# Optimization experiments

Hardware: AMD Instinct MI355X
Metric: run time of the kernel (lower is better)

Reference implementation:

```python
import jax, jax.numpy as jnp
import numpy as np

# SCOFFCell config (version=1, share_inp=True, step_att=True, LSTM, no rel-memory)
NUM_HIDDEN = 8      # number of object files (blocks)
SINGLE = 128        # single_hidden_size = hidden // num_hidden
N_TEMPLATES = 4     # schemata
COMM_HEADS = 4
D_KC = 32           # comm attn d_k = d_v
D_KI = 64           # input attn d_k
TOPK = 5            # topkval: active blocks
TAU = 0.5           # gumbel-softmax temperature for template selection
BS, NUM_INPUTS, INPUT_SIZE = 2048, 8, 128
HIDDEN = NUM_HIDDEN * SINGLE


def setup_inputs() -> dict:
    key = jax.random.key(0)
    ks = jax.random.split(key, 20)
    s = 0.05
    n = lambda k, shape, sc=s: jax.random.normal(k, shape, jnp.float32) * sc
    return {
        'inp': jax.random.normal(ks[0], (BS, NUM_INPUTS, INPUT_SIZE), jnp.float32),
        'hx': jax.random.normal(ks[1], (BS, HIDDEN), jnp.float32),
        'cx': jax.random.normal(ks[2], (BS, HIDDEN), jnp.float32),
        # input attention (shared across blocks, skip_write -> no output proj)
        'Wq_i': n(ks[3], (SINGLE, D_KI)),
        'Wk_i': n(ks[4], (INPUT_SIZE, D_KI)),
        'Wv_i': n(ks[5], (INPUT_SIZE, SINGLE)),
        # communication attention
        'Wq_c': n(ks[6], (SINGLE, COMM_HEADS * D_KC)),
        'Wk_c': n(ks[7], (SINGLE, COMM_HEADS * D_KC)),
        'Wv_c': n(ks[8], (SINGLE, COMM_HEADS * D_KC)),
        'Wf_c': n(ks[9], (COMM_HEADS * D_KC, SINGLE)),
        'bf_c': jnp.zeros((SINGLE,), jnp.float32),
        'Wg_c': n(ks[10], (COMM_HEADS * D_KC, SINGLE)),
        'bg_c': jnp.zeros((SINGLE,), jnp.float32),
        # SharedBlockLSTM: n_templates LSTMCells (torch gate order i,f,g,o)
        'W_ih': n(ks[11], (N_TEMPLATES, 4 * SINGLE, SINGLE)),
        'W_hh': n(ks[12], (N_TEMPLATES, 4 * SINGLE, SINGLE)),
        'b_ih': jnp.zeros((N_TEMPLATES, 4 * SINGLE), jnp.float32),
        'b_hh': jnp.zeros((N_TEMPLATES, 4 * SINGLE), jnp.float32),
        # template read/write keys
        'W_read': n(ks[13], (SINGLE, 16)),
        'W_write': n(ks[14], (N_TEMPLATES, SINGLE, 16)),
    }


def _scoff_forward(inp, hx, cx, Wq_i, Wk_i, Wv_i, Wq_c, Wk_c, Wv_c, Wf_c, bf_c,
                   Wg_c, bg_c, W_ih, W_hh, b_ih, b_hh, W_read, W_write):
    bs = inp.shape[0]
    k, sh = NUM_HIDDEN, SINGLE
    # ---- input attention: each block's hx chunk queries [slots ++ null-slot] ----
    kv = jnp.concatenate([inp, jnp.zeros_like(inp[:, :1])], axis=1)  # [bs, n_in+1, d_in]
    q = hx.reshape(bs, k, sh)
    qs = q @ Wq_i                                     # [bs, k, d_ki]
    ksl = kv @ Wk_i                                   # [bs, n_in+1, d_ki]
    vs = kv @ Wv_i                                    # [bs, n_in+1, sh]
    iatt = jax.nn.softmax(jnp.einsum('bkd,bnd->bkn', qs, ksl) / jnp.sqrt(jnp.float32(D_KI)), axis=-1)
    inp_use = jnp.einsum('bkn,bnd->bkd', iatt, vs).reshape(bs, k * sh)
    # ---- top-k block mask: zero the (k - topkval) blocks with largest iatt[:,:,0] ----
    n_drop = k - TOPK
    _, drop_idx = jax.lax.top_k(iatt[:, :, 0], n_drop)
    new_mask = jnp.ones((bs, k), inp.dtype).at[jnp.arange(bs)[:, None], drop_idx].set(0.0)
    mask_b = jax.lax.stop_gradient(new_mask)          # mask.detach()
    block_mask = mask_b[:, :, None]                   # [bs, k, 1]
    mask = jnp.repeat(block_mask, sh, axis=2).reshape(bs, k * sh)
    # ---- SharedBlockLSTM: run all templates, gumbel-ST select per block ----
    x = inp_use.reshape(bs * k, sh)
    h = hx.reshape(bs * k, sh)
    c = cx.reshape(bs * k, sh)
    gates = (jnp.einsum('ni,mgi->nmg', x, W_ih) + jnp.einsum('ni,mgi->nmg', h, W_hh)
             + b_ih + b_hh)                           # [N, m, 4*sh]
    i_g, f_g, g_g, o_g = jnp.split(gates, 4, axis=-1)
    c_t = jax.nn.sigmoid(f_g) * c[:, None, :] + jax.nn.sigmoid(i_g) * jnp.tanh(g_g)  # [N, m, sh]
    h_t = jax.nn.sigmoid(o_g) * jnp.tanh(c_t)
    h_read = h @ W_read                               # [N, 16]
    write_key = jnp.einsum('nms,msd->nmd', h_t, W_write)  # [N, m, 16]
    logits = jnp.einsum('nd,nmd->nm', h_read, write_key)
    gkey = jax.random.fold_in(jax.random.key(0), 12345)
    gumb = jax.random.gumbel(gkey, logits.shape, logits.dtype)
    y_soft = jax.nn.softmax((logits + gumb) / TAU, axis=-1)
    y_hard = jax.nn.one_hot(jnp.argmax(y_soft, axis=-1), N_TEMPLATES, dtype=y_soft.dtype)
    att = y_soft + jax.lax.stop_gradient(y_hard - y_soft)  # straight-through gumbel
    hx_new = jnp.einsum('nm,nms->ns', att, h_t).reshape(bs, k * sh)
    cx_new = jnp.einsum('nm,nms->ns', att, c_t).reshape(bs, k * sh)
    temp_att = att.reshape(bs, k, N_TEMPLATES)
    # ---- communication attention over blocks (blocked_grad masking) ----
    hb = hx_new.reshape(bs, k, sh)
    m3 = mask.reshape(bs, k, sh)
    hbg = m3 * hb + jax.lax.stop_gradient((1.0 - m3) * hb)  # fwd identity, bwd grad*mask
    heads = lambda t, W: (t @ W).reshape(bs, k, COMM_HEADS, D_KC).transpose(0, 2, 1, 3)
    qc, kc, vc = heads(hbg, Wq_c), heads(hbg, Wk_c), heads(hbg, Wv_c)
    catt = jax.nn.softmax(jnp.einsum('bhqd,bhkd->bhqk', qc, kc) / jnp.sqrt(jnp.float32(D_KC)), axis=-1)
    o = jnp.einsum('bhqk,bhkd->bhqd', catt, vc).transpose(0, 2, 1, 3).reshape(bs, k, COMM_HEADS * D_KC)
    comm = jax.nn.sigmoid(o @ Wg_c + bg_c) * jnp.tanh(o @ Wf_c + bf_c)  # gated residual update
    hx_new = (hb + comm).reshape(bs, k * sh)
    # ---- write back only active blocks ----
    hx_out = mask * hx_new + (1.0 - mask) * hx
    cx_out = mask * cx_new + (1.0 - mask) * cx
    return hx_out, cx_out, mask, block_mask, temp_att


def reference(inp, hx, cx, Wq_i, Wk_i, Wv_i, Wq_c, Wk_c, Wv_c, Wf_c, bf_c,
              Wg_c, bg_c, W_ih, W_hh, b_ih, b_hh, W_read, W_write):
    return _scoff_forward(inp, hx, cx, Wq_i, Wk_i, Wv_i, Wq_c, Wk_c, Wv_c, Wf_c,
                          bf_c, Wg_c, bg_c, W_ih, W_hh, b_ih, b_hh, W_read, W_write)
```

## Files before the change

### kernel.cpp

```cpp
#include <hip/hip_runtime.h>
#include <hip/hip_bf16.h>
#include <stdint.h>

typedef __hip_bfloat16 bf16;
typedef _Float16 half_t;
typedef __attribute__((ext_vector_type(8))) _Float16 half8;
typedef __attribute__((ext_vector_type(4))) float float4v;

struct TF2 { unsigned a, b; };
__host__ __device__ constexpr unsigned rotl32(unsigned v, int r) {
  return (v << r) | (v >> (32 - r));
}
__host__ __device__ constexpr TF2 tf2x32(unsigned k0, unsigned k1, unsigned x0, unsigned x1) {
  unsigned ks2 = k0 ^ k1 ^ 0x1BD11BDAu;
  x0 += k0; x1 += k1;
  const int ra[4] = {13, 15, 26, 6};
  const int rb[4] = {17, 29, 16, 24};
  for (int i = 0; i < 4; i++) { x0 += x1; x1 = rotl32(x1, ra[i]); x1 ^= x0; }
  x0 += k1; x1 += ks2 + 1u;
  for (int i = 0; i < 4; i++) { x0 += x1; x1 = rotl32(x1, rb[i]); x1 ^= x0; }
  x0 += ks2; x1 += k0 + 2u;
  for (int i = 0; i < 4; i++) { x0 += x1; x1 = rotl32(x1, ra[i]); x1 ^= x0; }
  x0 += k0; x1 += k1 + 3u;
  for (int i = 0; i < 4; i++) { x0 += x1; x1 = rotl32(x1, rb[i]); x1 ^= x0; }
  x0 += k1; x1 += ks2 + 4u;
  for (int i = 0; i < 4; i++) { x0 += x1; x1 = rotl32(x1, ra[i]); x1 ^= x0; }
  x0 += ks2; x1 += k0 + 5u;
  return TF2{x0, x1};
}
constexpr unsigned GK0 = tf2x32(0u, 0u, 0u, 12345u).a;
constexpr unsigned GK1 = tf2x32(0u, 0u, 0u, 12345u).b;

__device__ __forceinline__ float gumbel_at(unsigned j) {
  TF2 r = tf2x32(GK0, GK1, 0u, j);
  unsigned bits = r.a ^ r.b;
  float u = __uint_as_float((bits >> 9) | 0x3f800000u) - 1.0f;
  u = fmaxf(1.17549435e-38f, u + 1.17549435e-38f);
  return -logf(-logf(u));
}

__device__ __forceinline__ float sigm(float x) { return 1.0f / (1.0f + expf(-x)); }

#define MFMA16(a, b, c) __builtin_amdgcn_mfma_f32_16x16x32_f16((a), (b), (c), 0, 0, 0)

constexpr int GH  = 0;
constexpr int GL  = 524288;
constexpr int WWH = 1048576;
constexpr int WWL = 1056768;
constexpr int CQ  = 1064960;
constexpr int CF  = 1114112;
constexpr int CG  = 1130496;
constexpr int WS_HALF_TOTAL = 1146880;
constexpr size_t WS_FLAG_OFF = (size_t)WS_HALF_TOTAL * 2;
constexpr size_t WS_NEED     = WS_FLAG_OFF + 64;

constexpr size_t F_GH  = 0;
constexpr size_t F_GL  = 524288;
constexpr size_t F_WWH = 1048576;
constexpr size_t F_WWL = 1056768;
constexpr size_t F_CQ  = 1064960;
constexpr size_t F_XH  = 1146880;
constexpr size_t F_XL  = 5341184;
constexpr size_t F_HB  = 9535488;
constexpr size_t F_END = 11632640;
constexpr size_t G_HREAD = 0;
constexpr size_t G_MASK8 = 262144;
constexpr size_t G_FLAG  = 278528;
constexpr size_t WS2_NEED = F_END * 2 + (G_FLAG + 16) * 4;

__global__ void k_detect(const void* inp, int* flag) {
  __shared__ int bad;
  if (threadIdx.x == 0) bad = 0;
  __syncthreads();
  const unsigned short* u = (const unsigned short*)inp;
  for (int i = threadIdx.x; i < 1024; i += 256) {
    float v = __uint_as_float(((unsigned)u[i]) << 16);
    if (!(fabsf(v) < 64.f)) atomicOr(&bad, 1);
  }
  __syncthreads();
  if (threadIdx.x == 0) *flag = bad ? 0 : 1;
}

__global__ __launch_bounds__(256)
void k_wsplit2(const int* __restrict__ flag,
               const float* __restrict__ W_ih, const float* __restrict__ W_hh,
               const float* __restrict__ W_write,
               const float* __restrict__ Wq_c, const float* __restrict__ Wk_c,
               const float* __restrict__ Wv_c, const float* __restrict__ Wf_c,
               const float* __restrict__ Wg_c, half_t* __restrict__ ws) {
  if (*flag != 0) return;
  int tid = blockIdx.x * 256 + threadIdx.x;
  if (tid < 65536) {
    int m = tid >> 14, nt = (tid >> 9) & 31, ks = (tid >> 6) & 7, lane = tid & 63;
    int n = m * 512 + nt * 16 + (lane & 15);
    int kb = ks * 32 + (lane >> 4) * 8;
    half8 hi, lo;
#pragma unroll
    for (int j = 0; j < 8; j++) {
      int k = kb + j;
      float w = (k < 128) ? W_ih[n * 128 + k] : W_hh[n * 128 + (k - 128)];
      half_t h = (half_t)w;
      hi[j] = h; lo[j] = (half_t)(w - (float)h);
    }
    *reinterpret_cast<half8*>(ws + F_GH + (size_t)tid * 8) = hi;
    *reinterpret_cast<half8*>(ws + F_GL + (size_t)tid * 8) = lo;
  } else if (tid < 73728) {
    int j = tid - 65536; int md = j >> 7, s = j & 127; int m = md >> 4, d = md & 15;
    float w = W_write[(m * 128 + s) * 16 + d];
    half_t h = (half_t)w;
    ws[F_WWH + j] = h;
    ws[F_WWL + j] = (half_t)(w - (float)h);
  } else if (tid < 83968) {
    int u = tid - 73728;
    int which = u >> 11, r8 = u & 2047;
    int col = r8 >> 4, k8 = r8 & 15;
    const float* Wsel = which == 0 ? Wq_c : which == 1 ? Wk_c :
                        which == 2 ? Wv_c : which == 3 ? Wf_c : Wg_c;
    half8 v;
#pragma unroll
    for (int j = 0; j < 8; j++) v[j] = (half_t)Wsel[(k8 * 8 + j) * 128 + col];
    *reinterpret_cast<half8*>(ws + F_CQ + (size_t)which * 16384 + col * 128 + k8 * 8) = v;
  }
}

__global__ __launch_bounds__(256)
void kA(const int* __restrict__ flag,
        const float* __restrict__ inp, const float* __restrict__ hx,
        const float* __restrict__ Wq_i, const float* __restrict__ Wk_i,
        const float* __restrict__ Wv_i, const float* __restrict__ W_read,
        half_t* __restrict__ xh, half_t* __restrict__ xl,
        float* __restrict__ hread, float* __restrict__ mask8,
        float* __restrict__ out_mask, float* __restrict__ out_bm)
{
  if (*flag != 0) return;
  const int t = threadIdx.x;
  const int n0 = blockIdx.x * 16, gbase = n0 * 128;
  __shared__ __align__(16) float inps[2048], hxs[2048], vsb[2048];
  __shared__ float qsb[1088], kslb[1088];
  __shared__ float Xf[2112];
  __shared__ float attb[160];
  __shared__ float m8_[16];

  for (int idx = t; idx < 512; idx += 256) {
    *reinterpret_cast<float4*>(&hxs[idx * 4]) =
        *reinterpret_cast<const float4*>(hx + gbase + idx * 4);
    *reinterpret_cast<float4*>(&inps[idx * 4]) =
        *reinterpret_cast<const float4*>(inp + gbase + idx * 4);
  }
  __syncthreads();
  for (int idx = t; idx < 1024; idx += 256) {
    int k16 = idx >> 6, d = idx & 63;
    float aq = 0.f, ak = 0.f;
#pragma unroll 8
    for (int i = 0; i < 128; i++) {
      aq += hxs[k16 * 128 + i]  * Wq_i[i * 64 + d];
      ak += inps[k16 * 128 + i] * Wk_i[i * 64 + d];
    }
    qsb[k16 * 68 + d] = aq; kslb[k16 * 68 + d] = ak;
  }
  for (int idx = t; idx < 2048; idx += 256) {
    int n16 = idx >> 7, j = idx & 127;
    float a = 0.f;
#pragma unroll 8
    for (int i = 0; i < 128; i++) a += inps[n16 * 128 + i] * Wv_i[i * 128 + j];
    vsb[idx] = a;
  }
  {
    int n16 = t >> 4, d = t & 15;
    float a = 0.f;
#pragma unroll 8
    for (int i = 0; i < 128; i++) a += hxs[n16 * 128 + i] * W_read[i * 16 + d];
    hread[(size_t)(n0 + n16) * 16 + d] = a;
  }
  __syncthreads();
  if (t < 128) {
    int b2 = t >> 6, k = (t >> 3) & 7, n = t & 7;
    float sc = 0.f;
#pragma unroll
    for (int d = 0; d < 64; d++)
      sc += qsb[(b2 * 8 + k) * 68 + d] * kslb[(b2 * 8 + n) * 68 + d];
    attb[b2 * 72 + k * 9 + n] = sc * 0.125f;
  } else if (t < 144) {
    int u = t - 128, b2 = u >> 3, k = u & 7;
    attb[b2 * 72 + k * 9 + 8] = 0.f;
  }
  __syncthreads();
  if (t < 16) {
    int b2 = t >> 3, k = t & 7;
    float* row = &attb[b2 * 72 + k * 9];
    float mx = row[0];
    for (int n = 1; n < 9; n++) mx = fmaxf(mx, row[n]);
    float e[9], ssum = 0.f;
    for (int n = 0; n < 9; n++) { e[n] = expf(row[n] - mx); ssum += e[n]; }
    for (int n = 0; n < 9; n++) row[n] = e[n] / ssum;
  }
  __syncthreads();
  if (t < 2) {
    bool taken[8] = {};
    for (int dd = 0; dd < 3; dd++) {
      int bi = 0; float bv = -1e30f;
      for (int k = 0; k < 8; k++) {
        float v = attb[t * 72 + k * 9 + 0];
        if (!taken[k] && v > bv) { bv = v; bi = k; }
      }
      taken[bi] = true;
    }
    for (int k = 0; k < 8; k++) m8_[t * 8 + k] = taken[k] ? 0.f : 1.f;
  }
  __syncthreads();
  for (int idx = t; idx < 2048; idx += 256) {
    int n16 = idx >> 7, j = idx & 127, b2 = n16 >> 3, k = n16 & 7;
    float a = 0.f;
#pragma unroll
    for (int n = 0; n < 8; n++) a += attb[b2 * 72 + k * 9 + n] * vsb[(b2 * 8 + n) * 128 + j];
    Xf[n16 * 132 + j] = a;
    out_mask[gbase + idx] = m8_[n16];
  }
  if (t < 16) { out_bm[n0 + t] = m8_[t]; mask8[n0 + t] = m8_[t]; }
  __syncthreads();
  for (int u = t; u < 512; u += 256) {
    int ks = u >> 6, lane = u & 63, c15 = lane & 15, qd = lane >> 4;
    int kb = ks * 32 + qd * 8;
    half8 hi, lo;
#pragma unroll
    for (int j = 0; j < 8; j++) {
      int k = kb + j;
      float v = (k < 128) ? Xf[c15 * 132 + k] : hxs[c15 * 128 + (k - 128)];
      half_t h = (half_t)v;
      hi[j] = h; lo[j] = (half_t)(v - (float)h);
    }
    size_t off = ((size_t)(blockIdx.x * 8 + ks) * 64 + lane) * 8;
    *reinterpret_cast<half8*>(xh + off) = hi;
    *reinterpret_cast<half8*>(xl + off) = lo;
  }
}

__global__ __launch_bounds__(512, 2)
void kB(const int* __restrict__ flag, const half_t* __restrict__ wsp,
        const float* __restrict__ cx,
        const float* __restrict__ b_ih, const float* __restrict__ b_hh,
        const float* __restrict__ hread, const float* __restrict__ mask8,
        half_t* __restrict__ hbout, float* __restrict__ out_cx,
        float* __restrict__ out_ta)
{
  if (*flag != 0) return;
  const int t = threadIdx.x, lane = t & 63, w = t >> 6;
  const int m = w >> 1, sh = w & 1;
  const int c15 = lane & 15, qd = lane >> 4;
  const int n0 = blockIdx.x * 32;

  __shared__ __align__(16) half_t hth[32 * 520];
  __shared__ __align__(16) half_t htl[32 * 520];
  __shared__ float wks[2048];
  __shared__ float zb[128];
  __shared__ float m8s[32];
  __shared__ int msh[32];

  if (t < 32) m8s[t] = mask8[n0 + t];

  float4v acc[16][2];
#pragma unroll
  for (int ct = 0; ct < 16; ct++)
#pragma unroll
    for (int mt = 0; mt < 2; mt++) acc[ct][mt] = (float4v){0.f, 0.f, 0.f, 0.f};

  const half_t* xh = wsp + F_XH;
  const half_t* xl = wsp + F_XL;
  for (int ks = 0; ks < 8; ks++) {
    half8 ah[2], al[2];
#pragma unroll
    for (int mt = 0; mt < 2; mt++) {
      size_t aoff = ((size_t)((blockIdx.x * 2 + mt) * 8 + ks) * 64 + lane) * 8;
      ah[mt] = *reinterpret_cast<const half8*>(xh + aoff);
      al[mt] = *reinterpret_cast<const half8*>(xl + aoff);
    }
#pragma unroll
    for (int ct = 0; ct < 16; ct++) {
      int nt = (ct >> 2) * 8 + sh * 4 + (ct & 3);
      size_t boff = ((size_t)((m * 32 + nt) * 8 + ks) * 64 + lane) * 8;
      half8 bh = *reinterpret_cast<const half8*>(wsp + F_GH + boff);
      half8 bl = *reinterpret_cast<const half8*>(wsp + F_GL + boff);
#pragma unroll
      for (int mt = 0; mt < 2; mt++) {
        acc[ct][mt] = MFMA16(ah[mt], bh, acc[ct][mt]);
        acc[ct][mt] = MFMA16(ah[mt], bl, acc[ct][mt]);
        acc[ct][mt] = MFMA16(al[mt], bh, acc[ct][mt]);
      }
    }
  }
  float ccr[4][2][4];
#pragma unroll
  for (int c4 = 0; c4 < 4; c4++) {
    int s = sh * 64 + c4 * 16 + c15;
    float bi = b_ih[m * 512 + s]       + b_hh[m * 512 + s];
    float bf = b_ih[m * 512 + 128 + s] + b_hh[m * 512 + 128 + s];
    float bg = b_ih[m * 512 + 256 + s] + b_hh[m * 512 + 256 + s];
    float bo = b_ih[m * 512 + 384 + s] + b_hh[m * 512 + 384 + s];
#pragma unroll
    for (int mt = 0; mt < 2; mt++) {
#pragma unroll
      for (int rg = 0; rg < 4; rg++) {
        int row = mt * 16 + qd * 4 + rg;
        float iv = acc[c4][mt][rg]      + bi;
        float fv = acc[4 + c4][mt][rg]  + bf;
        float gv = acc[8 + c4][mt][rg]  + bg;
        float ov = acc[12 + c4][mt][rg] + bo;
        float cxv = cx[(size_t)(n0 + row) * 128 + s];
        float cc = sigm(fv) * cxv + sigm(iv) * tanhf(gv);
        float hh = sigm(ov) * tanhf(cc);
        ccr[c4][mt][rg] = cc;
        half_t hhi = (half_t)hh;
        hth[row * 520 + m * 128 + s] = hhi;
        htl[row * 520 + m * 128 + s] = (half_t)(hh - (float)hhi);
      }
    }
  }
  __syncthreads();
  {
    float4v wa = (float4v){0.f, 0.f, 0.f, 0.f};
    const half_t* Wh = wsp + F_WWH + (m * 16 + c15) * 128 + qd * 8;
    const half_t* Wl = wsp + F_WWL + (m * 16 + c15) * 128 + qd * 8;
    const half_t* Hh = &hth[(sh * 16 + c15) * 520 + m * 128 + qd * 8];
    const half_t* Hl = &htl[(sh * 16 + c15) * 520 + m * 128 + qd * 8];
#pragma unroll
    for (int ks = 0; ks < 4; ks++) {
      half8 ahf = *reinterpret_cast<const half8*>(Hh + ks * 32);
      half8 alf = *reinterpret_cast<const half8*>(Hl + ks * 32);
      half8 bhf = *reinterpret_cast<const half8*>(Wh + ks * 32);
      half8 blf = *reinterpret_cast<const half8*>(Wl + ks * 32);
      wa = MFMA16(ahf, bhf, wa);
      wa = MFMA16(ahf, blf, wa);
      wa = MFMA16(alf, bhf, wa);
    }
#pragma unroll
    for (int rg = 0; rg < 4; rg++)
      wks[m * 512 + (sh * 16 + qd * 4 + rg) * 16 + c15] = wa[rg];
  }
  __syncthreads();
  if (t < 128) {
    int row = t >> 2, mm = t & 3;
    float lg = 0.f;
#pragma unroll
    for (int d = 0; d < 16; d++)
      lg += hread[(size_t)(n0 + row) * 16 + d] * wks[mm * 512 + row * 16 + d];
    zb[t] = lg + gumbel_at((unsigned)((n0 + row) * 4 + mm));
  }
  __syncthreads();
  if (t < 32) {
    int ms = 0; float best = zb[t * 4];
#pragma unroll
    for (int mm = 1; mm < 4; mm++)
      if (zb[t * 4 + mm] > best) { best = zb[t * 4 + mm]; ms = mm; }
    msh[t] = ms;
#pragma unroll
    for (int mm = 0; mm < 4; mm++)
      out_ta[(size_t)(n0 + t) * 4 + mm] = (mm == ms) ? 1.0f : 0.0f;
  }
  __syncthreads();
#pragma unroll
  for (int c4 = 0; c4 < 4; c4++) {
    int s = sh * 64 + c4 * 16 + c15;
#pragma unroll
    for (int mt = 0; mt < 2; mt++) {
#pragma unroll
      for (int rg = 0; rg < 4; rg++) {
        int row = mt * 16 + qd * 4 + rg;
        if (msh[row] == m) {
          float co = (m8s[row] != 0.f) ? ccr[c4][mt][rg]
                                       : cx[(size_t)(n0 + row) * 128 + s];
          out_cx[(size_t)(n0 + row) * 128 + s] = co;
        }
      }
    }
  }
  for (int idx = t; idx < 4096; idx += 512) {
    int r = idx >> 7, s = idx & 127;
    hbout[(size_t)(n0 + r) * 128 + s] = hth[r * 520 + msh[r] * 128 + s];
  }
}

__global__ __launch_bounds__(256)
void kC(const int* __restrict__ flag, const half_t* __restrict__ wsp,
        const half_t* __restrict__ hbin, const float* __restrict__ mask8,
        const float* __restrict__ hx,
        const float* __restrict__ bf_c, const float* __restrict__ bg_c,
        float* __restrict__ out_hx)
{
  if (*flag != 0) return;
  const int t = threadIdx.x;
  const int n0 = blockIdx.x * 16;
  const int lane = t & 63, wv = t >> 6;
  const int col15 = lane & 15, quad = lane >> 4;

  __shared__ __align__(16) half_t hbF[2176], qcF[2176], kcF[2176], vcF[2176], oF[2176];
  __shared__ float attb[512];
  __shared__ float m8s[16];

  {
    int r = t >> 4, c8 = t & 15;
    *reinterpret_cast<half8*>(&hbF[r * 136 + c8 * 8]) =
        *reinterpret_cast<const half8*>(hbin + (size_t)(n0 + r) * 128 + c8 * 8);
  }
  if (t < 16) m8s[t] = mask8[n0 + t];
  __syncthreads();

  if (wv < 3) {
    float4v pacc[8];
#pragma unroll
    for (int ct = 0; ct < 8; ct++) pacc[ct] = (float4v){0.f, 0.f, 0.f, 0.f};
    const half_t* Bp = wsp + F_CQ + wv * 16384 + col15 * 128 + quad * 8;
    const half_t* Ap = &hbF[col15 * 136 + quad * 8];
#pragma unroll
    for (int ks = 0; ks < 4; ks++) {
      half8 a = *reinterpret_cast<const half8*>(Ap + ks * 32);
#pragma unroll
      for (int ct = 0; ct < 8; ct++) {
        half8 b = *reinterpret_cast<const half8*>(Bp + ct * 2048 + ks * 32);
        pacc[ct] = MFMA16(a, b, pacc[ct]);
      }
    }
    half_t* dst = (wv == 0) ? qcF : (wv == 1) ? kcF : vcF;
#pragma unroll
    for (int ct = 0; ct < 8; ct++)
#pragma unroll
      for (int rg = 0; rg < 4; rg++)
        dst[(quad * 4 + rg) * 136 + ct * 16 + col15] = (half_t)pacc[ct][rg];
  }
  __syncthreads();

  if (t < 64) {
    int b2 = t >> 5, h = (t >> 3) & 3, q = t & 7;
    float sc[8];
#pragma unroll
    for (int kq = 0; kq < 8; kq++) {
      float a = 0.f;
#pragma unroll
      for (int d = 0; d < 32; d++)
        a += (float)qcF[(b2 * 8 + q) * 136 + h * 32 + d] *
             (float)kcF[(b2 * 8 + kq) * 136 + h * 32 + d];
      sc[kq] = a * 0.17677669529663688110f;
    }
    float mx = sc[0];
#pragma unroll
    for (int kq = 1; kq < 8; kq++) mx = fmaxf(mx, sc[kq]);
    float e[8], ssum = 0.f;
#pragma unroll
    for (int kq = 0; kq < 8; kq++) { e[kq] = expf(sc[kq] - mx); ssum += e[kq]; }
#pragma unroll
    for (int kq = 0; kq < 8; kq++)
      attb[((b2 * 4 + h) * 8 + q) * 8 + kq] = e[kq] / ssum;
  }
  __syncthreads();

  for (int idx = t; idx < 2048; idx += 256) {
    int r = idx >> 7, cn = idx & 127, b2 = r >> 3, q = r & 7, h = cn >> 5;
    float a = 0.f;
#pragma unroll
    for (int kq = 0; kq < 8; kq++)
      a += attb[((b2 * 4 + h) * 8 + q) * 8 + kq] * (float)vcF[(b2 * 8 + kq) * 136 + cn];
    oF[r * 136 + cn] = (half_t)a;
  }
  __syncthreads();

  {
    float4v fa[2], ga[2];
#pragma unroll
    for (int tt = 0; tt < 2; tt++) {
      fa[tt] = (float4v){0.f, 0.f, 0.f, 0.f};
      ga[tt] = (float4v){0.f, 0.f, 0.f, 0.f};
    }
    const half_t* Ao = &oF[col15 * 136 + quad * 8];
    const half_t* Bf = wsp + F_CQ + 3 * 16384 + (wv * 32 + col15) * 128 + quad * 8;
    const half_t* Bg = wsp + F_CQ + 4 * 16384 + (wv * 32 + col15) * 128 + quad * 8;
#pragma unroll
    for (int ks = 0; ks < 4; ks++) {
      half8 a = *reinterpret_cast<const half8*>(Ao + ks * 32);
#pragma unroll
      for (int tt = 0; tt < 2; tt++) {
        half8 bfv = *reinterpret_cast<const half8*>(Bf + tt * 2048 + ks * 32);
        half8 bgv = *reinterpret_cast<const half8*>(Bg + tt * 2048 + ks * 32);
        fa[tt] = MFMA16(a, bfv, fa[tt]);
        ga[tt] = MFMA16(a, bgv, ga[tt]);
      }
    }
#pragma unroll
    for (int tt = 0; tt < 2; tt++) {
      int col = wv * 32 + tt * 16 + col15;
      float bfb = bf_c[col], bgb = bg_c[col];
#pragma unroll
      for (int rg = 0; rg < 4; rg++) {
        int row = quad * 4 + rg;
        float af = fa[tt][rg] + bfb;
        float ag = ga[tt][rg] + bgb;
        float comm = sigm(ag) * tanhf(af);
        float hbv = (float)hbF[row * 136 + col];
        float hv = (m8s[row] != 0.f) ? (hbv + comm)
                                     : hx[(size_t)(n0 + row) * 128 + col];
        out_hx[(size_t)(n0 + row) * 128 + col] = hv;
      }
    }
  }
}

__global__ __launch_bounds__(256)
void k_wsplit(const float* __restrict__ W_ih, const float* __restrict__ W_hh,
              const float* __restrict__ W_write,
              const float* __restrict__ Wq_c, const float* __restrict__ Wk_c,
              const float* __restrict__ Wv_c, const float* __restrict__ Wf_c,
              const float* __restrict__ Wg_c, half_t* __restrict__ ws) {
  int i = blockIdx.x * 256 + threadIdx.x;
  if (i < 524288) {
    int n = i >> 8, k = i & 255;
    int m = n >> 9, g = n & 511;
    float w = (k < 128) ? W_ih[(m * 512 + g) * 128 + k]
                        : W_hh[(m * 512 + g) * 128 + (k - 128)];
    half_t h = (half_t)w;
    ws[GH + i] = h;
    ws[GL + i] = (half_t)(w - (float)h);
  } else if (i < 532480) {
    int j = i - 524288; int md = j >> 7, s = j & 127; int m = md >> 4, d = md & 15;
    float w = W_write[(m * 128 + s) * 16 + d];
    half_t h = (half_t)w;
    ws[WWH + j] = h;
    ws[WWL + j] = (half_t)(w - (float)h);
  } else if (i < 614400) {
    int j = i - 532480; int which = j >> 14, r = j & 16383;
    int col = r >> 7, k = r & 127;
    const float* Wsel = which == 0 ? Wq_c : which == 1 ? Wk_c :
                        which == 2 ? Wv_c : which == 3 ? Wf_c : Wg_c;
    ws[CQ + which * 16384 + r] = (half_t)Wsel[k * 128 + col];
  }
}

__global__ __launch_bounds__(256)
void k_scoff_mfma(const int* __restrict__ flag, const half_t* __restrict__ wsp,
                  const float* __restrict__ inp, const float* __restrict__ hx,
                  const float* __restrict__ cx,
                  const float* __restrict__ Wq_i, const float* __restrict__ Wk_i,
                  const float* __restrict__ Wv_i,
                  const float* __restrict__ bf_c, const float* __restrict__ bg_c,
                  const float* __restrict__ b_ih, const float* __restrict__ b_hh,
                  const float* __restrict__ W_read,
                  float* __restrict__ out_hx, float* __restrict__ out_cx,
                  float* __restrict__ out_mask, float* __restrict__ out_bm,
                  float* __restrict__ out_ta)
{
  if (*flag != 0) return;

  const int t = threadIdx.x;
  const int n0 = blockIdx.x * 16, gbase = n0 * 128;
  const int lane = t & 63, wv = t >> 6;
  const int col15 = lane & 15, quad = lane >> 4;

  __shared__ __align__(16) float hxs[2048];
  __shared__ __align__(16) float cxs[2048];
  __shared__ __align__(16) float vsb[2048];
  __shared__ float qsb[1088], kslb[1088];
  __shared__ __align__(16) half_t sXh[16 * 264];
  __shared__ __align__(16) half_t sXl[16 * 264];
  __shared__ __align__(16) half_t hth[16 * 520];
  __shared__ __align__(16) half_t htl[16 * 520];
  __shared__ __align__(16) half_t cts[16 * 512];
  __shared__ float wks[1024];
  __shared__ __align__(16) half_t hbF[16 * 136];
  __shared__ __align__(16) half_t oF[16 * 136];
  __shared__ __align__(16) half_t qcF[16 * 136];
  __shared__ __align__(16) half_t kcF[16 * 136];
  __shared__ __align__(16) half_t vcF[16 * 136];
  __shared__ float attb[512];
  __shared__ float hrs_[256];
  __shared__ float zbuf[64];
  __shared__ float m8_[16];
  __shared__ int   msh_[16];

  for (int idx = t; idx < 512; idx += 256) {
    *reinterpret_cast<float4*>(&hxs[idx * 4]) =
        *reinterpret_cast<const float4*>(hx + gbase + idx * 4);
    *reinterpret_cast<float4*>(&cxs[idx * 4]) =
        *reinterpret_cast<const float4*>(cx + gbase + idx * 4);
  }
  {
    __shared__ __align__(16) float inps[2048];
    for (int idx = t; idx < 512; idx += 256)
      *reinterpret_cast<float4*>(&inps[idx * 4]) =
          *reinterpret_cast<const float4*>(inp + gbase + idx * 4);
    __syncthreads();
    for (int idx = t; idx < 1024; idx += 256) {
      int k16 = idx >> 6, d = idx & 63;
      float aq = 0.f, ak = 0.f;
#pragma unroll 8
      for (int i = 0; i < 128; i++) {
        aq += hxs[k16 * 128 + i]  * Wq_i[i * 64 + d];
        ak += inps[k16 * 128 + i] * Wk_i[i * 64 + d];
      }
      qsb[k16 * 68 + d] = aq; kslb[k16 * 68 + d] = ak;
    }
    for (int idx = t; idx < 2048; idx += 256) {
      int n16 = idx >> 7, j = idx & 127;
      float a = 0.f;
#pragma unroll 8
      for (int i = 0; i < 128; i++) a += inps[n16 * 128 + i] * Wv_i[i * 128 + j];
      vsb[idx] = a;
    }
  }
  {
    int n16 = t >> 4, d = t & 15;
    float a = 0.f;
#pragma unroll 8
    for (int i = 0; i < 128; i++) a += hxs[n16 * 128 + i] * W_read[i * 16 + d];
    hrs_[t] = a;
  }
  for (int idx = t; idx < 2048; idx += 256) {
    int r = idx >> 7, i = idx & 127;
    float v = hxs[r * 128 + i];
    half_t hh = (half_t)v;
    sXh[r * 264 + 128 + i] = hh;
    sXl[r * 264 + 128 + i] = (half_t)(v - (float)hh);
  }
  __syncthreads();

  if (t < 128) {
    int b2 = t >> 6, k = (t >> 3) & 7, n = t & 7;
    float sc = 0.f;
#pragma unroll
    for (int d = 0; d < 64; d++)
      sc += qsb[(b2 * 8 + k) * 68 + d] * kslb[(b2 * 8 + n) * 68 + d];
    attb[b2 * 72 + k * 9 + n] = sc * 0.125f;
  } else if (t < 144) {
    int u = t - 128, b2 = u >> 3, k = u & 7;
    attb[b2 * 72 + k * 9 + 8] = 0.f;
  }
  __syncthreads();
  if (t < 16) {
    int b2 = t >> 3, k = t & 7;
    float* row = &attb[b2 * 72 + k * 9];
    float mx = row[0];
    for (int n = 1; n < 9; n++) mx = fmaxf(mx, row[n]);
    float e[9], ssum = 0.f;
    for (int n = 0; n < 9; n++) { e[n] = expf(row[n] - mx); ssum += e[n]; }
    for (int n = 0; n < 9; n++) row[n] = e[n] / ssum;
  }
  __syncthreads();
  if (t < 2) {
    bool taken[8] = {};
    for (int dd = 0; dd < 3; dd++) {
      int bi = 0; float bv = -1e30f;
      for (int k = 0; k < 8; k++) {
        float v = attb[t * 72 + k * 9 + 0];
        if (!taken[k] && v > bv) { bv = v; bi = k; }
      }
      taken[bi] = true;
    }
    for (int k = 0; k < 8; k++) m8_[t * 8 + k] = taken[k] ? 0.f : 1.f;
  }
  __syncthreads();
  for (int idx = t; idx < 2048; idx += 256) {
    int n16 = idx >> 7, j = idx & 127, b2 = n16 >> 3, k = n16 & 7;
    float a = 0.f;
#pragma unroll
    for (int n = 0; n < 8; n++) a += attb[b2 * 72 + k * 9 + n] * vsb[(b2 * 8 + n) * 128 + j];
    half_t hh = (half_t)a;
    sXh[n16 * 264 + j] = hh;
    sXl[n16 * 264 + j] = (half_t)(a - (float)hh);
    out_mask[gbase + idx] = m8_[n16];
  }
  if (t < 16) out_bm[n0 + t] = m8_[t];
  __syncthreads();
  for (int idx = t; idx < 2048; idx += 256) vsb[idx] = b_ih[idx] + b_hh[idx];
  __syncthreads();

  {
// ... 634 lines not shown
```

Baseline: 367.3 us.

## Loop LSTM gate MFMA per column chunk and split scalar projection accumulators

The LSTM gate GEMM no longer keeps all 16x2 accumulator tiles live at once. It loops over four column chunks, each holding only its four gate tiles, and runs the gate nonlinearity right after that chunk's GEMM. This cuts VGPR pressure to allow more waves per CU, at the cost of reloading the X operand fragments once per chunk. The saved cell state is now kept in fp16 registers, which loses precision in out_cx. The scalar Q/K/V/read projection loops also use four independent accumulators each, to break the serial FMA dependency chain.

```diff
diff --git a/kernel.cpp b/kernel.cpp
--- a/kernel.cpp
+++ b/kernel.cpp
@@ -150,27 +150,45 @@
   __syncthreads();
   for (int idx = t; idx < 1024; idx += 256) {
     int k16 = idx >> 6, d = idx & 63;
-    float aq = 0.f, ak = 0.f;
+    float aq0 = 0.f, aq1 = 0.f, aq2 = 0.f, aq3 = 0.f;
+    float ak0 = 0.f, ak1 = 0.f, ak2 = 0.f, ak3 = 0.f;
 #pragma unroll 8
-    for (int i = 0; i < 128; i++) {
-      aq += hxs[k16 * 128 + i]  * Wq_i[i * 64 + d];
-      ak += inps[k16 * 128 + i] * Wk_i[i * 64 + d];
-    }
-    qsb[k16 * 68 + d] = aq; kslb[k16 * 68 + d] = ak;
+    for (int i = 0; i < 128; i += 4) {
+      aq0 += hxs[k16 * 128 + i]     * Wq_i[i * 64 + d];
+      aq1 += hxs[k16 * 128 + i + 1] * Wq_i[(i + 1) * 64 + d];
+      aq2 += hxs[k16 * 128 + i + 2] * Wq_i[(i + 2) * 64 + d];
+      aq3 += hxs[k16 * 128 + i + 3] * Wq_i[(i + 3) * 64 + d];
+      ak0 += inps[k16 * 128 + i]     * Wk_i[i * 64 + d];
+      ak1 += inps[k16 * 128 + i + 1] * Wk_i[(i + 1) * 64 + d];
+      ak2 += inps[k16 * 128 + i + 2] * Wk_i[(i + 2) * 64 + d];
+      ak3 += inps[k16 * 128 + i + 3] * Wk_i[(i + 3) * 64 + d];
+    }
+    qsb[k16 * 68 + d]  = (aq0 + aq1) + (aq2 + aq3);
+    kslb[k16 * 68 + d] = (ak0 + ak1) + (ak2 + ak3);
   }
   for (int idx = t; idx < 2048; idx += 256) {
     int n16 = idx >> 7, j = idx & 127;
-    float a = 0.f;
+    float a0 = 0.f, a1 = 0.f, a2 = 0.f, a3 = 0.f;
 #pragma unroll 8
-    for (int i = 0; i < 128; i++) a += inps[n16 * 128 + i] * Wv_i[i * 128 + j];
-    vsb[idx] = a;
+    for (int i = 0; i < 128; i += 4) {
+      a0 += inps[n16 * 128 + i]     * Wv_i[i * 128 + j];
+      a1 += inps[n16 * 128 + i + 1] * Wv_i[(i + 1) * 128 + j];
+      a2 += inps[n16 * 128 + i + 2] * Wv_i[(i + 2) * 128 + j];
+      a3 += inps[n16 * 128 + i + 3] * Wv_i[(i + 3) * 128 + j];
+    }
+    vsb[idx] = (a0 + a1) + (a2 + a3);
   }
   {
     int n16 = t >> 4, d = t & 15;
-    float a = 0.f;
+    float a0 = 0.f, a1 = 0.f, a2 = 0.f, a3 = 0.f;
 #pragma unroll 8
-    for (int i = 0; i < 128; i++) a += hxs[n16 * 128 + i] * W_read[i * 16 + d];
-    hread[(size_t)(n0 + n16) * 16 + d] = a;
+    for (int i = 0; i < 128; i += 4) {
+      a0 += hxs[n16 * 128 + i]     * W_read[i * 16 + d];
+      a1 += hxs[n16 * 128 + i + 1] * W_read[(i + 1) * 16 + d];
+      a2 += hxs[n16 * 128 + i + 2] * W_read[(i + 2) * 16 + d];
+      a3 += hxs[n16 * 128 + i + 3] * W_read[(i + 3) * 16 + d];
+    }
+    hread[(size_t)(n0 + n16) * 16 + d] = (a0 + a1) + (a2 + a3);
   }
   __syncthreads();
   if (t < 128) {
@@ -258,39 +276,43 @@
 
   if (t < 32) m8s[t] = mask8[n0 + t];
 
-  float4v acc[16][2];
-#pragma unroll
-  for (int ct = 0; ct < 16; ct++)
-#pragma unroll
-    for (int mt = 0; mt < 2; mt++) acc[ct][mt] = (float4v){0.f, 0.f, 0.f, 0.f};
-
   const half_t* xh = wsp + F_XH;
   const half_t* xl = wsp + F_XL;
-  for (int ks = 0; ks < 8; ks++) {
-    half8 ah[2], al[2];
-#pragma unroll
-    for (int mt = 0; mt < 2; mt++) {
-      size_t aoff = ((size_t)((blockIdx.x * 2 + mt) * 8 + ks) * 64 + lane) * 8;
-      ah[mt] = *reinterpret_cast<const half8*>(xh + aoff);
-      al[mt] = *reinterpret_cast<const half8*>(xl + aoff);
-    }
-#pragma unroll
-    for (int ct = 0; ct < 16; ct++) {
-      int nt = (ct >> 2) * 8 + sh * 4 + (ct & 3);
-      size_t boff = ((size_t)((m * 32 + nt) * 8 + ks) * 64 + lane) * 8;
-      half8 bh = *reinterpret_cast<const half8*>(wsp + F_GH + boff);
-      half8 bl = *reinterpret_cast<const half8*>(wsp + F_GL + boff);
+
+  half_t ccr[4][2][4];
+
+  for (int c4 = 0; c4 < 4; c4++) {
+    float4v acc[4][2];
+#pragma unroll
+    for (int g = 0; g < 4; g++)
+#pragma unroll
+      for (int mt = 0; mt < 2; mt++) acc[g][mt] = (float4v){0.f, 0.f, 0.f, 0.f};
+
+    for (int ks = 0; ks < 8; ks++) {
+      half8 ah[2], al[2];
 #pragma unroll
       for (int mt = 0; mt < 2; mt++) {
-        acc[ct][mt] = MFMA16(ah[mt], bh, acc[ct][mt]);
-        acc[ct][mt] = MFMA16(ah[mt], bl, acc[ct][mt]);
-        acc[ct][mt] = MFMA16(al[mt], bh, acc[ct][mt]);
-      }
-    }
-  }
-  float ccr[4][2][4];
-#pragma unroll
-  for (int c4 = 0; c4 < 4; c4++) {
+        size_t aoff = ((size_t)((blockIdx.x * 2 + mt) * 8 + ks) * 64 + lane) * 8;
+        ah[mt] = *reinterpret_cast<const half8*>(xh + aoff);
+        al[mt] = *reinterpret_cast<const half8*>(xl + aoff);
+      }
+      half8 bh[4], bl[4];
+#pragma unroll
+      for (int g = 0; g < 4; g++) {
+        int nt = g * 8 + sh * 4 + c4;
+        size_t boff = ((size_t)((m * 32 + nt) * 8 + ks) * 64 + lane) * 8;
+        bh[g] = *reinterpret_cast<const half8*>(wsp + F_GH + boff);
+        bl[g] = *reinterpret_cast<const half8*>(wsp + F_GL + boff);
+      }
+#pragma unroll
+      for (int g = 0; g < 4; g++)
+#pragma unroll
+        for (int mt = 0; mt < 2; mt++) {
+          acc[g][mt] = MFMA16(ah[mt], bh[g], acc[g][mt]);
+          acc[g][mt] = MFMA16(ah[mt], bl[g], acc[g][mt]);
+          acc[g][mt] = MFMA16(al[mt], bh[g], acc[g][mt]);
+        }
+    }
     int s = sh * 64 + c4 * 16 + c15;
     float bi = b_ih[m * 512 + s]       + b_hh[m * 512 + s];
     float bf = b_ih[m * 512 + 128 + s] + b_hh[m * 512 + 128 + s];
@@ -301,14 +323,14 @@
 #pragma unroll
       for (int rg = 0; rg < 4; rg++) {
         int row = mt * 16 + qd * 4 + rg;
-        float iv = acc[c4][mt][rg]      + bi;
-        float fv = acc[4 + c4][mt][rg]  + bf;
-        float gv = acc[8 + c4][mt][rg]  + bg;
-        float ov = acc[12 + c4][mt][rg] + bo;
+        float iv = acc[0][mt][rg] + bi;
+        float fv = acc[1][mt][rg] + bf;
+        float gv = acc[2][mt][rg] + bg;
+        float ov = acc[3][mt][rg] + bo;
         float cxv = cx[(size_t)(n0 + row) * 128 + s];
         float cc = sigm(fv) * cxv + sigm(iv) * tanhf(gv);
         float hh = sigm(ov) * tanhf(cc);
-        ccr[c4][mt][rg] = cc;
+        ccr[c4][mt][rg] = (half_t)cc;
         half_t hhi = (half_t)hh;
         hth[row * 520 + m * 128 + s] = hhi;
         htl[row * 520 + m * 128 + s] = (half_t)(hh - (float)hhi);
@@ -366,7 +388,7 @@
       for (int rg = 0; rg < 4; rg++) {
         int row = mt * 16 + qd * 4 + rg;
         if (msh[row] == m) {
-          float co = (m8s[row] != 0.f) ? ccr[c4][mt][rg]
+          float co = (m8s[row] != 0.f) ? (float)ccr[c4][mt][rg]
                                        : cx[(size_t)(n0 + row) * 128 + s];
           out_cx[(size_t)(n0 + row) * 128 + s] = co;
         }
```

After: 308.0 us. -16.1%, faster.
